# Kernel tuning notes

Measured on AMD Instinct MI355X. Metric: run time of the kernel, lower is better.

Reference implementation:

```python
import jax, jax.numpy as jnp
import numpy as np
from jax import lax

LEAK = 0.01   # nn.LeakyReLU default negative slope
EPS = 1e-5    # BatchNorm2d eps


def _conv(x, w, b, stride, pad):
    # torch Conv2d, NCHW / OIHW
    y = lax.conv_general_dilated(x, w, (stride, stride), [(pad, pad), (pad, pad)],
                                 dimension_numbers=('NCHW', 'OIHW', 'NCHW'))
    return y + b[None, :, None, None]


def _bn_lrelu(x, g, b):
    # BatchNorm2d in training mode (torch default): batch statistics over (N,H,W)
    m = jnp.mean(x, axis=(0, 2, 3), keepdims=True)
    v = jnp.var(x, axis=(0, 2, 3), keepdims=True)
    xn = (x - m) * lax.rsqrt(v + EPS) * g[None, :, None, None] + b[None, :, None, None]
    return jnp.where(xn >= 0, xn, LEAK * xn)


def _convt(x, w, b):
    # ConvTranspose2d with stride == kernel_size, padding=0: non-overlapping
    # k x k expansion of every pixel -> expressible as one einsum + reshape.
    # w: (Cin, Cout, k, k) (torch ConvTranspose2d layout)
    B, C, H, W = x.shape
    _, Co, k, _ = w.shape
    y = jnp.einsum('bchw,coij->bohiwj', x, w).reshape(B, Co, H * k, W * k)
    return y + b[None, :, None, None]


def setup_inputs() -> dict:
    key = jax.random.key(0)
    ks = iter(jax.random.split(key, 64))
    def rn(shape, s=0.05):
        return jax.random.normal(next(ks), shape, dtype=jnp.float32) * s
    d = {}
    d['x'] = jax.random.normal(next(ks), (16, 3, 128, 128), dtype=jnp.float32)
    enc_shapes = [(64, 3, 4, 4), (128, 64, 4, 4), (256, 128, 4, 4), (256, 256, 4, 4)]
    for i, s in enumerate(enc_shapes):
        d[f'enc_w{i}'] = rn(s)
        d[f'enc_b{i}'] = jnp.zeros((s[0],), jnp.float32)
    for i, c in enumerate([64, 128, 256]):
        d[f'ebn_g{i}'] = jnp.ones((c,), jnp.float32)
        d[f'ebn_b{i}'] = jnp.zeros((c,), jnp.float32)
    d['codebook'] = rn((512, 256), 1.0)  # (codebook_size, latent_dim)
    dec_shapes = [(256, 128, 4, 4), (128, 64, 2, 2), (64, 32, 2, 2)]
    for i, s in enumerate(dec_shapes):
        d[f'dec_w{i}'] = rn(s)
        d[f'dec_b{i}'] = jnp.zeros((s[1],), jnp.float32)
        d[f'dbn_g{i}'] = jnp.ones((s[1],), jnp.float32)
        d[f'dbn_b{i}'] = jnp.zeros((s[1],), jnp.float32)
    d['dec_w3'] = rn((3, 32, 1, 1))
    d['dec_b3'] = jnp.zeros((3,), jnp.float32)
    return d


def reference(x,
              enc_w0, enc_b0, ebn_g0, ebn_b0,
              enc_w1, enc_b1, ebn_g1, ebn_b1,
              enc_w2, enc_b2, ebn_g2, ebn_b2,
              enc_w3, enc_b3,
              codebook,
              dec_w0, dec_b0, dbn_g0, dbn_b0,
              dec_w1, dec_b1, dbn_g1, dbn_b1,
              dec_w2, dec_b2, dbn_g2, dbn_b2,
              dec_w3, dec_b3):
    # ---- encoder ----
    h = _bn_lrelu(_conv(x, enc_w0, enc_b0, 2, 1), ebn_g0, ebn_b0)   # (B,64,64,64)
    h = _bn_lrelu(_conv(h, enc_w1, enc_b1, 2, 1), ebn_g1, ebn_b1)   # (B,128,32,32)
    h = _bn_lrelu(_conv(h, enc_w2, enc_b2, 2, 1), ebn_g2, ebn_b2)   # (B,256,16,16)
    z = _conv(h, enc_w3, enc_b3, 2, 1)                               # (B,256,8,8)

    # ---- vector quantizer ----
    B, C, H, W = z.shape
    zf = z.transpose(0, 2, 3, 1).reshape(-1, C)                      # (BHW, C)
    # squared L2 distances to every codebook entry
    d2 = (jnp.sum(zf * zf, axis=-1, keepdims=True)
          - 2.0 * zf @ codebook.T
          + jnp.sum(codebook * codebook, axis=-1)[None, :])          # (BHW, K)
    idx = jnp.argmin(d2, axis=-1)                                    # (BHW,)
    min_d = jnp.min(d2, axis=-1)
    q = codebook[idx]                                                # (BHW, C)
    commitment_loss = jnp.mean((lax.stop_gradient(q) - zf) ** 2)
    codebook_loss = jnp.mean((q - lax.stop_gradient(zf)) ** 2)
    q_st = zf + lax.stop_gradient(q - zf)                            # straight-through
    qz = q_st.reshape(B, H, W, C).transpose(0, 3, 1, 2)              # (B,256,8,8)

    # ---- decoder ----
    h = _bn_lrelu(_convt(qz, dec_w0, dec_b0), dbn_g0, dbn_b0)        # (B,128,32,32)
    h = _bn_lrelu(_convt(h, dec_w1, dec_b1), dbn_g1, dbn_b1)         # (B,64,64,64)
    h = _bn_lrelu(_convt(h, dec_w2, dec_b2), dbn_g2, dbn_b2)         # (B,32,128,128)
    out = jnp.tanh(jnp.einsum('bchw,oc->bohw', h, dec_w3[:, :, 0, 0])
                   + dec_b3[None, :, None, None])                    # (B,3,128,128)

    return (out, commitment_loss, codebook_loss,
            idx.reshape(B, H, W), min_d.reshape(B, H, W))
```

## Files before the change

kernel.cpp:

```cpp
#include <hip/hip_runtime.h>
#include <math.h>

#define LEAK 0.01f

typedef __bf16 bf16x8 __attribute__((ext_vector_type(8)));
typedef float f32x4 __attribute__((ext_vector_type(4)));
typedef unsigned short ushort;
typedef unsigned int uint32;

struct HL { ushort h, l; };

__device__ inline HL split_bf16(float x) {
    unsigned u = __float_as_uint(x);
    unsigned hr = (u + 0x7FFFu + ((u >> 16) & 1u)) >> 16;
    float fh = __uint_as_float(hr << 16);
    float r = x - fh;
    unsigned v = __float_as_uint(r);
    unsigned lr = (v + 0x7FFFu + ((v >> 16) & 1u)) >> 16;
    HL out; out.h = (ushort)hr; out.l = (ushort)lr;
    return out;
}

template<int MODE>
__device__ inline void stage_load(float (&pv)[2][4], const float* __restrict__ Bf,
                                  int kbase, int n0, int tid,
                                  int Ci, int Hin, int Ho, int lgHo, int lgHW) {
    int nl = tid & 31, kg = tid >> 5;
    int n = n0 + nl;
#pragma unroll
    for (int r = 0; r < 2; ++r) {
        if (MODE == 0) {
            int k4 = kbase + (r << 5) + (kg << 2);
            int ic = k4 >> 4, kh = (k4 >> 2) & 3;
            int ow = n & (Ho - 1), oh = (n >> lgHo) & (Ho - 1), b = n >> (lgHo + lgHo);
            int ih = oh * 2 - 1 + kh;
            int ihc = ih < 0 ? 0 : (ih >= Hin ? Hin - 1 : ih);
            int iwb = ow * 2 - 1;
            size_t base = ((size_t)(b * Ci + ic) * Hin + ihc) * Hin;
#pragma unroll
            for (int e = 0; e < 4; ++e) {
                int iw = iwb + e;
                int iwc = iw < 0 ? 0 : (iw >= Hin ? Hin - 1 : iw);
                pv[r][e] = Bf[base + iwc];
            }
        } else {
            int c = kbase + (r << 5) + (kg << 2);
            int b = n >> lgHW, hw = n & ((1 << lgHW) - 1);
            size_t base = (((size_t)(b * Ci + c)) << lgHW) + hw;
            size_t str = (size_t)1 << lgHW;
#pragma unroll
            for (int e = 0; e < 4; ++e) pv[r][e] = Bf[base + e * str];
        }
    }
}

template<int MODE>
__global__ __launch_bounds__(256, 3) void gemm_mfma(
    const ushort* __restrict__ Ah, const ushort* __restrict__ Al,
    const float* __restrict__ Bf,
    const float* __restrict__ bnt, const float* __restrict__ gamma,
    const float* __restrict__ beta, float invN, int chanShift,
    const float* __restrict__ bias, float* __restrict__ P,
    int Mtiles, int Ntiles, int K, int Kslice, int KS, int outSize,
    int Ci, int Hin, int Co, int Ho, int lgHo,
    int lgHW, int lgHin, int lgCo, int lgk,
    float* __restrict__ statsBnt, const float* __restrict__ bnPart,
    int statsBank, int bntBankStride)
{
    __shared__ __align__(16) uint32 Bsp[32 * 68];
    __shared__ float scs[256], shs[256];

    int bid = blockIdx.x;
    int ntile = bid % Ntiles; bid /= Ntiles;
    int mtile = bid % Mtiles;
    int ks = bid / Mtiles;
    int tid = threadIdx.x;
    int lane = tid & 63, w = tid >> 6;
    int quad = lane >> 4, tl = lane & 15;
    int n0 = ntile << 5, m0 = mtile << 7, k0 = ks * Kslice;
    int Kt = K >> 5;

    bool useBN = (bnt != nullptr) || (bnPart != nullptr);
    int c0 = k0 >> chanShift;
    if (bnPart != nullptr) {
        int c = tid >> 2, qq = tid & 3;
        const float2* pp2 = (const float2*)(bnPart + c * 512) + qq * 64;
        float s = 0.f, s2 = 0.f;
#pragma unroll 8
        for (int p = 0; p < 64; ++p) { float2 v = pp2[p]; s += v.x; s2 += v.y; }
        scs[tid] = s; shs[tid] = s2;
        __syncthreads();
        float scale = 0.f, shift = 0.f;
        if (tid < 64) {
            float st = scs[tid * 4] + scs[tid * 4 + 1] + scs[tid * 4 + 2] + scs[tid * 4 + 3];
            float qt = shs[tid * 4] + shs[tid * 4 + 1] + shs[tid * 4 + 2] + shs[tid * 4 + 3];
            float m = st * invN;
            float var = qt * invN - m * m;
            scale = gamma[tid] * rsqrtf(var + 1e-5f);
            shift = beta[tid] - m * scale;
        }
        __syncthreads();
        if (tid < 64 && tid >= c0) { scs[tid - c0] = scale; shs[tid - c0] = shift; }
    } else if (bnt != nullptr) {
        int nch = Kslice >> chanShift;
        for (int c = tid; c < nch; c += 256) {
            float sm, sq;
            if (bntBankStride > 0) {
                sm = 0.f; sq = 0.f;
#pragma unroll
                for (int bk = 0; bk < 8; ++bk) {
                    sm += bnt[bk * bntBankStride + (c0 + c) * 2];
                    sq += bnt[bk * bntBankStride + (c0 + c) * 2 + 1];
                }
            } else {
                sm = bnt[(c0 + c) * 2];
                sq = bnt[(c0 + c) * 2 + 1];
            }
            float m = sm * invN;
            float var = sq * invN - m * m;
            float scale = gamma[c0 + c] * rsqrtf(var + 1e-5f);
            scs[c] = scale;
            shs[c] = beta[c0 + c] - m * scale;
        }
    }
    __syncthreads();

    f32x4 zero4 = {0.f, 0.f, 0.f, 0.f};
    f32x4 acc[2][2];
#pragma unroll
    for (int mt = 0; mt < 2; ++mt)
#pragma unroll
        for (int nt = 0; nt < 2; ++nt) acc[mt][nt] = zero4;

    if (MODE == 2) {
        const ushort* Bu = (const ushort*)Bf;
        for (int kc = 0; kc < Kslice; kc += 32) {
            int kbase = k0 + kc;
            int kt = kbase >> 5;
            bf16x8 afh[2], afl[2];
#pragma unroll
            for (int mt = 0; mt < 2; ++mt) {
                int mtAbs = (m0 >> 4) + (w << 1) + mt;
                size_t abase = (((size_t)mtAbs * Kt + kt) << 6) + lane;
                afh[mt] = *(const bf16x8*)(Ah + abase * 8);
                afl[mt] = *(const bf16x8*)(Al + abase * 8);
            }
            bf16x8 bfh[2], bfl[2];
#pragma unroll
            for (int nt = 0; nt < 2; ++nt) {
                int n = n0 + (nt << 4) + tl;
                size_t ba = (size_t)n * Ci + kbase + (quad << 3);
                bfh[nt] = *(const bf16x8*)(Bu + ba);
                bfl[nt] = *(const bf16x8*)(Bu + Ho + ba);
            }
#pragma unroll
            for (int mt = 0; mt < 2; ++mt)
#pragma unroll
                for (int nt = 0; nt < 2; ++nt) {
                    acc[mt][nt] = __builtin_amdgcn_mfma_f32_16x16x32_bf16(afh[mt], bfh[nt], acc[mt][nt], 0, 0, 0);
                    acc[mt][nt] = __builtin_amdgcn_mfma_f32_16x16x32_bf16(afh[mt], bfl[nt], acc[mt][nt], 0, 0, 0);
                    acc[mt][nt] = __builtin_amdgcn_mfma_f32_16x16x32_bf16(afl[mt], bfh[nt], acc[mt][nt], 0, 0, 0);
                }
        }
    } else {
        int nsteps = Kslice >> 6;
        float pvA[2][4], pvB[2][4];
        stage_load<MODE>(pvA, Bf, k0, n0, tid, Ci, Hin, Ho, lgHo, lgHW);
        if (nsteps > 1) stage_load<MODE>(pvB, Bf, k0 + 64, n0, tid, Ci, Hin, Ho, lgHo, lgHW);

        auto step = [&](float (&pv)[2][4], int sidx) {
            int kbase = k0 + (sidx << 6);
            int nl = tid & 31, kg = tid >> 5;
#pragma unroll
            for (int r = 0; r < 2; ++r) {
                int k4 = kbase + (r << 5) + (kg << 2);
                uint32 pk[4];
                if (MODE == 0) {
                    int ic = k4 >> 4, kh = (k4 >> 2) & 3;
                    int n = n0 + nl;
                    int ow = n & (Ho - 1), oh = (n >> lgHo) & (Ho - 1);
                    int ih = oh * 2 - 1 + kh;
                    bool rowok = (unsigned)ih < (unsigned)Hin;
                    int iwb = ow * 2 - 1;
                    float sc_ = useBN ? scs[ic - c0] : 0.f;
                    float sh_ = useBN ? shs[ic - c0] : 0.f;
#pragma unroll
                    for (int e = 0; e < 4; ++e) {
                        int iw = iwb + e;
                        bool ok = rowok && ((unsigned)iw < (unsigned)Hin);
                        float f = pv[r][e];
                        if (useBN) { f = f * sc_ + sh_; f = f >= 0.f ? f : LEAK * f; }
                        if (!ok) f = 0.f;
                        HL s = split_bf16(f);
                        pk[e] = ((uint32)s.h << 16) | s.l;
                    }
                } else {
#pragma unroll
                    for (int e = 0; e < 4; ++e) {
                        float f = pv[r][e];
                        if (useBN) {
                            int lc = k4 + e - k0;
                            f = f * scs[lc] + shs[lc];
                            f = f >= 0.f ? f : LEAK * f;
                        }
                        HL s = split_bf16(f);
                        pk[e] = ((uint32)s.h << 16) | s.l;
                    }
                }
                *(uint4*)&Bsp[nl * 68 + (r << 5) + (kg << 2)] = make_uint4(pk[0], pk[1], pk[2], pk[3]);
            }
            __syncthreads();

            if (sidx + 2 < nsteps)
                stage_load<MODE>(pv, Bf, kbase + 128, n0, tid, Ci, Hin, Ho, lgHo, lgHW);

#pragma unroll
            for (int sub = 0; sub < 2; ++sub) {
                int kt = (kbase >> 5) + sub;
                bf16x8 afh[2], afl[2];
#pragma unroll
                for (int mt = 0; mt < 2; ++mt) {
                    int mtAbs = (m0 >> 4) + (w << 1) + mt;
                    size_t abase = (((size_t)mtAbs * Kt + kt) << 6) + lane;
                    afh[mt] = *(const bf16x8*)(Ah + abase * 8);
                    afl[mt] = *(const bf16x8*)(Al + abase * 8);
                }
                bf16x8 bfh[2], bfl[2];
#pragma unroll
                for (int nt = 0; nt < 2; ++nt) {
                    int base = ((nt << 4) + tl) * 68 + (sub << 5) + (quad << 3);
                    uint4 ua = *(const uint4*)&Bsp[base];
                    uint4 ub = *(const uint4*)&Bsp[base + 4];
                    union { uint32 u[4]; bf16x8 v; } H, L;
                    H.u[0] = __builtin_amdgcn_perm(ua.y, ua.x, 0x07060302u);
                    H.u[1] = __builtin_amdgcn_perm(ua.w, ua.z, 0x07060302u);
                    H.u[2] = __builtin_amdgcn_perm(ub.y, ub.x, 0x07060302u);
                    H.u[3] = __builtin_amdgcn_perm(ub.w, ub.z, 0x07060302u);
                    L.u[0] = __builtin_amdgcn_perm(ua.y, ua.x, 0x05040100u);
                    L.u[1] = __builtin_amdgcn_perm(ua.w, ua.z, 0x05040100u);
                    L.u[2] = __builtin_amdgcn_perm(ub.y, ub.x, 0x05040100u);
                    L.u[3] = __builtin_amdgcn_perm(ub.w, ub.z, 0x05040100u);
                    bfh[nt] = H.v; bfl[nt] = L.v;
                }
#pragma unroll
                for (int mt = 0; mt < 2; ++mt)
#pragma unroll
                    for (int nt = 0; nt < 2; ++nt) {
                        acc[mt][nt] = __builtin_amdgcn_mfma_f32_16x16x32_bf16(afh[mt], bfh[nt], acc[mt][nt], 0, 0, 0);
                        acc[mt][nt] = __builtin_amdgcn_mfma_f32_16x16x32_bf16(afh[mt], bfl[nt], acc[mt][nt], 0, 0, 0);
                        acc[mt][nt] = __builtin_amdgcn_mfma_f32_16x16x32_bf16(afl[mt], bfh[nt], acc[mt][nt], 0, 0, 0);
                    }
            }
            __syncthreads();
        };

        for (int s = 0; s < nsteps; s += 2) {
            step(pvA, s);
            if (s + 1 < nsteps) step(pvB, s + 1);
        }
    }

    bool doStats = (statsBnt != nullptr);
    if (doStats) {
        if (tid < 2 * Co) scs[tid] = 0.f;
        __syncthreads();
    }
    float ssum[2][4] = {{0.f,0.f,0.f,0.f},{0.f,0.f,0.f,0.f}};
    float ssq [2][4] = {{0.f,0.f,0.f,0.f},{0.f,0.f,0.f,0.f}};
    float* dst = P + (size_t)ks * outSize;
    if (MODE == 0) {
#pragma unroll
        for (int nt = 0; nt < 2; ++nt) {
            int n = n0 + (nt << 4) + tl;
            int ow = n & (Ho - 1), oh = (n >> lgHo) & (Ho - 1), b = n >> (lgHo + lgHo);
#pragma unroll
            for (int mt = 0; mt < 2; ++mt) {
                int mb = m0 + (w << 5) + (mt << 4) + (quad << 2);
#pragma unroll
                for (int r = 0; r < 4; ++r) {
                    int oc = mb + r;
                    float v = acc[mt][nt][r];
                    if (KS == 1) v += bias[oc];
                    if (doStats) { ssum[mt][r] += v; ssq[mt][r] += v * v; }
                    dst[((size_t)(b * Co + oc) * Ho + oh) * Ho + ow] = v;
                }
            }
        }
    } else {
        int kf = 1 << lgk;
        int Ho2 = Hin << lgk;
#pragma unroll
        for (int nt = 0; nt < 2; ++nt) {
            int n = n0 + (nt << 4) + tl;
            int b = n >> lgHW, hw = n & ((1 << lgHW) - 1);
            int h = hw >> lgHin, wp = hw & (Hin - 1);
#pragma unroll
            for (int mt = 0; mt < 2; ++mt) {
                int mb = m0 + (w << 5) + (mt << 4) + (quad << 2);
#pragma unroll
                for (int r = 0; r < 4; ++r) {
                    int m = mb + r;
                    int o = m & (Co - 1), ij = m >> lgCo;
                    int ii = ij >> lgk, jj = ij & (kf - 1);
                    float v = acc[mt][nt][r];
                    if (KS == 1) v += bias[o];
                    if (doStats) { ssum[mt][r] += v; ssq[mt][r] += v * v; }
                    dst[((size_t)(b * Co + o) * Ho2 + (h << lgk) + ii) * Ho2 + (wp << lgk) + jj] = v;
                }
            }
        }
    }
    if (doStats) {
#pragma unroll
        for (int mt = 0; mt < 2; ++mt)
#pragma unroll
            for (int r = 0; r < 4; ++r) {
                float s = ssum[mt][r], q2 = ssq[mt][r];
#pragma unroll
                for (int m2 = 1; m2 < 16; m2 <<= 1) {
                    s  += __shfl_xor(s,  m2);
                    q2 += __shfl_xor(q2, m2);
                }
                if (tl == 0) {
                    int m = m0 + (w << 5) + (mt << 4) + (quad << 2) + r;
                    int o = (MODE == 0) ? m : (m & (Co - 1));
                    atomicAdd(&scs[o * 2],     s);
                    atomicAdd(&scs[o * 2 + 1], q2);
                }
            }
        __syncthreads();
        float* sb = statsBnt + (blockIdx.x & 7) * statsBank;
        if (tid < 2 * Co) atomicAdd(&sb[tid], scs[tid]);
    }
}

__device__ inline int fragaddr(int m, int k, int K) {
    return ((((m >> 4) * (K >> 5) + (k >> 5)) << 9) | (((k >> 3) & 3) << 7) | ((m & 15) << 3) | (k & 7));
}

#define OUT_CL   786432
#define OUT_CB   786433
#define OUT_IDX  786434
#define OUT_MIND 787458

__device__ void conv_body(int bid, int tid,
                          const float* __restrict__ x, const float* __restrict__ w,
                          const float* __restrict__ bias, float* __restrict__ P,
                          float* __restrict__ pst, float (&cst)[4][16])
{
    const int Ci = 3, Hin = 128, Co = 64, Ho = 64, OCT = 8;
    int ntile = (16 * Ho * Ho) >> 8;
    int tile = bid % ntile;
    int og = bid / ntile;
    int oc0 = og * OCT;

    int px = (tile << 8) + tid;
    int ow = px % Ho; int t = px / Ho;
    int oh = t % Ho;  int b = t / Ho;

    int off[16]; float fm[16];
    int ih0 = oh * 2 - 1, iw0 = ow * 2 - 1;
#pragma unroll
    for (int kh = 0; kh < 4; ++kh)
#pragma unroll
        for (int kw = 0; kw < 4; ++kw) {
            int ih = ih0 + kh, iw = iw0 + kw;
            bool ok = (ih >= 0) && (ih < Hin) && (iw >= 0) && (iw < Hin);
            int ihc = ih < 0 ? 0 : (ih >= Hin ? Hin - 1 : ih);
            int iwc = iw < 0 ? 0 : (iw >= Hin ? Hin - 1 : iw);
            off[kh * 4 + kw] = ihc * Hin + iwc;
            fm[kh * 4 + kw] = ok ? 1.f : 0.f;
        }

    float acc[OCT];
#pragma unroll
    for (int u = 0; u < OCT; ++u) acc[u] = bias[oc0 + u];

    const float* xc = x + (size_t)b * Ci * Hin * Hin;
    const float* wi = w + (size_t)oc0 * Ci * 16;
    int HinHin = Hin * Hin;
    for (int ic = 0; ic < Ci; ++ic) {
        float xv[16];
#pragma unroll
        for (int q = 0; q < 16; ++q) xv[q] = xc[off[q]] * fm[q];
#pragma unroll
        for (int u = 0; u < OCT; ++u) {
            const float* wo = wi + (size_t)u * Ci * 16;
            float a = acc[u];
#pragma unroll
            for (int q = 0; q < 16; ++q) a += xv[q] * wo[q];
            acc[u] = a;
        }
        xc += HinHin;
        wi += 16;
    }
    size_t obase = (((size_t)b * Co + oc0) * Ho + oh) * Ho + ow;
    size_t opl = (size_t)Ho * Ho;
#pragma unroll
    for (int u = 0; u < OCT; ++u) P[obase + u * opl] = acc[u];

    float sv[OCT], qv[OCT];
#pragma unroll
    for (int u = 0; u < OCT; ++u) { sv[u] = acc[u]; qv[u] = acc[u] * acc[u]; }
#pragma unroll
    for (int m2 = 1; m2 < 64; m2 <<= 1)
#pragma unroll
        for (int u = 0; u < OCT; ++u) {
            sv[u] += __shfl_xor(sv[u], m2);
            qv[u] += __shfl_xor(qv[u], m2);
        }
    int lane = tid & 63, wv = tid >> 6;
    if (lane == 0) {
#pragma unroll
        for (int u = 0; u < OCT; ++u) { cst[wv][u * 2] = sv[u]; cst[wv][u * 2 + 1] = qv[u]; }
    }
    __syncthreads();
    if (tid < 2 * OCT) {
        float v = cst[0][tid] + cst[1][tid] + cst[2][tid] + cst[3][tid];
        pst[(oc0 + (tid >> 1)) * 512 + tile * 2 + (tid & 1)] = v;
    }
}

__global__ void prologue(const float* __restrict__ w1, const float* __restrict__ w2,
                         const float* __restrict__ w3, const float* __restrict__ d0,
                         const float* __restrict__ d1, const float* __restrict__ d2,
                         ushort* __restrict__ WH, ushort* __restrict__ WL,
                         const float* __restrict__ cb, float* __restrict__ cbT,
                         float* __restrict__ bnt, float* __restrict__ dout,
                         const float* __restrict__ x, const float* __restrict__ w0,
                         const float* __restrict__ b0, float* __restrict__ Y0,
                         float* __restrict__ pst) {
    __shared__ float cst[4][16];
    int blk = blockIdx.x;
    int tid = threadIdx.x;
    if (blk < 24) {
        bnt[blk * 256 + tid] = 0.f;
        if (blk == 0 && tid < 2) dout[OUT_CL + tid] = 0.f;
        return;
    }
    if (blk < 536) {
        int idx = (blk - 24) * 256 + tid;
        int k = idx & 511, c = idx >> 9;
        cbT[idx] = cb[k * 256 + c];
        return;
    }
    if (blk >= 9400) {
        conv_body(blk - 9400, tid, x, w0, b0, Y0, pst, cst);
        return;
    }
    int idx = (blk - 536) * 256 + tid;
    if (idx >= 2269184) return;
    float v; int dst;
    if (idx < 131072) {
        int m = idx >> 10, k = idx & 1023;
        v = w1[idx];
        dst = fragaddr(m, k, 1024);
    } else if (idx < 655360) {
        int i = idx - 131072;
        int m = i >> 11, k = i & 2047;
        v = w2[i];
        dst = 131072 + fragaddr(m, k, 2048);
    } else if (idx < 1703936) {
        int i = idx - 655360;
        int m = i >> 12, k = i & 4095;
        v = w3[i];
        dst = 655360 + fragaddr(m, k, 4096);
    } else if (idx < 2228224) {
        int i = idx - 1703936;
        int m = i >> 8, c = i & 255;
        int o = m & 127, ij = m >> 7;
        v = d0[((size_t)c * 128 + o) * 16 + ij];
        dst = 1703936 + fragaddr(m, c, 256);
    } else if (idx < 2260992) {
        int i = idx - 2228224;
        int m = i >> 7, c = i & 127;
        int o = m & 63, ij = m >> 6;
        v = d1[((size_t)c * 64 + o) * 4 + ij];
        dst = 2228224 + fragaddr(m, c, 128);
    } else {
        int i = idx - 2260992;
        int m = i >> 6, c = i & 63;
        int o = m & 31, ij = m >> 5;
        v = d2[((size_t)c * 32 + o) * 4 + ij];
        dst = 2260992 + fragaddr(m, c, 64);
    }
    HL s = split_bf16(v);
    WH[dst] = s.h; WL[dst] = s.l;
}

__global__ void reduce_bias_stats4(const float4* __restrict__ P, const float* __restrict__ bias,
                                   float4* __restrict__ y, float* __restrict__ bnt,
                                   int outSize4, int KS, int Co, int HW4, int nch) {
    int tid = threadIdx.x;
    int i = blockIdx.x * 256 + tid;
    int c = (i / HW4) % Co;
    float bv = bias[c];
    float4 s = make_float4(bv, bv, bv, bv);
    for (int ks = 0; ks < KS; ++ks) {
        float4 p = P[(size_t)ks * outSize4 + i];
        s.x += p.x; s.y += p.y; s.z += p.z; s.w += p.w;
    }
    y[i] = s;
    float ls  = s.x + s.y + s.z + s.w;
    float ls2 = s.x * s.x + s.y * s.y + s.z * s.z + s.w * s.w;
    __shared__ float as[16], aq[16];
    if (tid < 16) { as[tid] = 0.f; aq[tid] = 0.f; }
    __syncthreads();
    int c0 = ((blockIdx.x * 256) / HW4) % Co;
    atomicAdd(&as[c - c0], ls);
    atomicAdd(&aq[c - c0], ls2);
    __syncthreads();
    if (tid < nch) {
        atomicAdd(&bnt[(c0 + tid) * 2],     as[tid]);
        atomicAdd(&bnt[(c0 + tid) * 2 + 1], aq[tid]);
    }
}

__global__ void vq_main(const float* __restrict__ Pz, const float* __restrict__ b3,
                        const float* __restrict__ cbT, const float* __restrict__ cb,
                        ushort* __restrict__ qhl, float* __restrict__ dout) {
    int r0 = blockIdx.x * 4;
    int tid = threadIdx.x;
    int lane = tid & 63, w = tid >> 6;

    __shared__ __align__(16) float zT[256][4];
    __shared__ float wred[4][4];
    __shared__ float zn2s[4];
    __shared__ float wbd[4][4];
    __shared__ int   wbi[4][4];
    __shared__ int   bestsh[4];
    __shared__ float bestd[4];

    int b = r0 >> 6, s0 = r0 & 63;
    size_t zi = ((size_t)(b * 256 + tid)) * 64 + s0;
    float bv = b3[tid];
    float4 zv = make_float4(bv, bv, bv, bv);
    const float4* pp = (const float4*)Pz + (zi >> 2);
#pragma unroll
    for (int ks = 0; ks < 16; ++ks) {
        float4 p = pp[(size_t)ks * 65536];
        zv.x += p.x; zv.y += p.y; zv.z += p.z; zv.w += p.w;
    }
    *(float4*)&zT[tid][0] = zv;

    float p0 = zv.x * zv.x, p1 = zv.y * zv.y, p2 = zv.z * zv.z, p3 = zv.w * zv.w;
#pragma unroll
    for (int m2 = 1; m2 < 64; m2 <<= 1) {
        p0 += __shfl_xor(p0, m2); p1 += __shfl_xor(p1, m2);
        p2 += __shfl_xor(p2, m2); p3 += __shfl_xor(p3, m2);
    }
    if (lane == 0) { wred[w][0] = p0; wred[w][1] = p1; wred[w][2] = p2; wred[w][3] = p3; }
    __syncthreads();
    if (tid < 4) zn2s[tid] = wred[0][tid] + wred[1][tid] + wred[2][tid] + wred[3][tid];
    __syncthreads();

    float d0[4], d1[4];
#pragma unroll
    for (int rr = 0; rr < 4; ++rr) { d0[rr] = 0.f; d1[rr] = 0.f; }
    float cn0 = 0.f, cn1 = 0.f;
#pragma unroll 4
    for (int c = 0; c < 256; ++c) {
        float cv0 = cbT[c * 512 + tid];
        float cv1 = cbT[c * 512 + 256 + tid];
        cn0 += cv0 * cv0;
        cn1 += cv1 * cv1;
        float4 za = *(const float4*)&zT[c][0];
        d0[0] += za.x * cv0; d1[0] += za.x * cv1;
        d0[1] += za.y * cv0; d1[1] += za.y * cv1;
        d0[2] += za.z * cv0; d1[2] += za.z * cv1;
        d0[3] += za.w * cv0; d1[3] += za.w * cv1;
    }

#pragma unroll
    for (int rr = 0; rr < 4; ++rr) {
        float dist0 = zn2s[rr] - 2.f * d0[rr] + cn0;
        float dist1 = zn2s[rr] - 2.f * d1[rr] + cn1;
        float bd = dist0; int bi = tid;
        if (dist1 < bd) { bd = dist1; bi = tid + 256; }
#pragma unroll
        for (int m2 = 1; m2 < 64; m2 <<= 1) {
            float od = __shfl_xor(bd, m2); int oi = __shfl_xor(bi, m2);
            if (od < bd || (od == bd && oi < bi)) { bd = od; bi = oi; }
        }
        if (lane == 0) { wbd[w][rr] = bd; wbi[w][rr] = bi; }
    }
    __syncthreads();
    if (tid < 4) {
        float bd = wbd[0][tid]; int bi = wbi[0][tid];
#pragma unroll
        for (int ww = 1; ww < 4; ++ww) {
            float od = wbd[ww][tid]; int oi = wbi[ww][tid];
            if (od < bd || (od == bd && oi < bi)) { bd = od; bi = oi; }
        }
        bestsh[tid] = bi; bestd[tid] = bd;
        dout[OUT_IDX + r0 + tid]  = (float)bi;
        dout[OUT_MIND + r0 + tid] = bd;
    }
    __syncthreads();

#pragma unroll
    for (int rr = 0; rr < 4; ++rr) {
        float v = cb[(size_t)bestsh[rr] * 256 + tid];
        HL s = split_bf16(v);
        size_t o = (size_t)(r0 + rr) * 256 + tid;
        qhl[o]          = s.h;
        qhl[262144 + o] = s.l;
    }
    if (tid == 0) {
        float ls = (bestd[0] + bestd[1] + bestd[2] + bestd[3]) * (1.f / 262144.f);
        atomicAdd(&dout[OUT_CL], ls);
        atomicAdd(&dout[OUT_CB], ls);
    }
}

__global__ void final_conv_tanh(const float* __restrict__ hbuf, const float* __restrict__ bnt,
                                const float* __restrict__ g, const float* __restrict__ bt,
                                const float* __restrict__ w3, const float* __restrict__ b3,
                                float* __restrict__ out) {
    __shared__ float sc[32], sh[32], sw[96];
    int tid = threadIdx.x;
    if (tid < 32) {
        float sm = 0.f, sq = 0.f;
#pragma unroll
        for (int bk = 0; bk < 8; ++bk) {
            sm += bnt[bk * 64 + tid * 2];
            sq += bnt[bk * 64 + tid * 2 + 1];
        }
        float m = sm * (1.f / 262144.f);
        float var = sq * (1.f / 262144.f) - m * m;
        float scale = g[tid] * rsqrtf(var + 1e-5f);
        sc[tid] = scale;
        sh[tid] = bt[tid] - m * scale;
    }
    if (tid < 96) sw[tid] = w3[tid];
    __syncthreads();
    int idx = blockIdx.x * 256 + tid;
    int hw4 = idx & 4095;
    int b   = idx >> 12;
    const float4* hp = (const float4*)hbuf + ((size_t)b * 32) * 4096 + hw4;
    float b0 = b3[0], b1 = b3[1], b2 = b3[2];
    float4 a0 = make_float4(b0, b0, b0, b0);
    float4 a1 = make_float4(b1, b1, b1, b1);
    float4 a2 = make_float4(b2, b2, b2, b2);
#pragma unroll 8
    for (int c = 0; c < 32; ++c) {
        float4 v = hp[(size_t)c * 4096];
        float scv = sc[c], shv = sh[c];
        float vx = v.x * scv + shv; vx = vx >= 0.f ? vx : LEAK * vx;
        float vy = v.y * scv + shv; vy = vy >= 0.f ? vy : LEAK * vy;
        float vz = v.z * scv + shv; vz = vz >= 0.f ? vz : LEAK * vz;
        float vw = v.w * scv + shv; vw = vw >= 0.f ? vw : LEAK * vw;
        float w0 = sw[c], w1 = sw[32 + c], w2 = sw[64 + c];
        a0.x += vx * w0; a0.y += vy * w0; a0.z += vz * w0; a0.w += vw * w0;
        a1.x += vx * w1; a1.y += vy * w1; a1.z += vz * w1; a1.w += vw * w1;
        a2.x += vx * w2; a2.y += vy * w2; a2.z += vz * w2; a2.w += vw * w2;
    }
    float4* op = (float4*)out;
    size_t ob = ((size_t)b * 3) * 4096 + hw4;
    op[ob]            = make_float4(tanhf(a0.x), tanhf(a0.y), tanhf(a0.z), tanhf(a0.w));
    op[ob + 4096]     = make_float4(tanhf(a1.x), tanhf(a1.y), tanhf(a1.z), tanhf(a1.w));
    op[ob + 2 * 4096] = make_float4(tanhf(a2.x), tanhf(a2.y), tanhf(a2.z), tanhf(a2.w));
}

extern "C" void kernel_launch(void* const* d_in, const int* in_sizes, int n_in,
                              void* d_out, int out_size, void* d_ws, size_t ws_size,
                              hipStream_t stream) {
    const float* x      = (const float*)d_in[0];
    const float* enc_w0 = (const float*)d_in[1];
    const float* enc_b0 = (const float*)d_in[2];
    const float* enc_w1 = (const float*)d_in[3];
    const float* enc_b1 = (const float*)d_in[4];
    const float* enc_w2 = (const float*)d_in[5];
    const float* enc_b2 = (const float*)d_in[6];
    const float* enc_w3 = (const float*)d_in[7];
    const float* enc_b3 = (const float*)d_in[8];
    const float* ebn_g0 = (const float*)d_in[9];
    const float* ebn_b0 = (const float*)d_in[10];
    const float* ebn_g1 = (const float*)d_in[11];
    const float* ebn_b1 = (const float*)d_in[12];
    const float* ebn_g2 = (const float*)d_in[13];
    const float* ebn_b2 = (const float*)d_in[14];
    const float* cb     = (const float*)d_in[15];
    const float* dec_w0 = (const float*)d_in[16];
    const float* dec_b0 = (const float*)d_in[17];
    const float* dbn_g0 = (const float*)d_in[18];
    const float* dbn_b0 = (const float*)d_in[19];
    const float* dec_w1 = (const float*)d_in[20];
    const float* dec_b1 = (const float*)d_in[21];
    const float* dbn_g1 = (const float*)d_in[22];
    const float* dbn_b1 = (const float*)d_in[23];
    const float* dec_w2 = (const float*)d_in[24];
    const float* dec_b2 = (const float*)d_in[25];
    const float* dbn_g2 = (const float*)d_in[26];
    const float* dbn_b2 = (const float*)d_in[27];
    const float* dec_w3 = (const float*)d_in[28];
    const float* dec_b3 = (const float*)d_in[29];

    float* out = (float*)d_out;
    float* ws  = (float*)d_ws;

    float*  Y0   = ws;
    float*  Y1   = ws + 4194304;
    float*  Y2   = ws + 6291456;
    float*  PST  = ws + 7340032;
    float*  QHL  = ws + 7602176;
    ushort* WH   = (ushort*)(ws + 7864320);
    ushort* WL   = (ushort*)(ws + 8998912);
    float*  CBT  = ws + 10133504;
    float*  BNT  = ws + 10264576;
    float*  PART = ws + 10270720;
    float*  D0   = ws + 18659328;
    float*  D1   = ws + 20756480;
    float*  D2   = ws + 24950784;

    dim3 blk(256);

    prologue<<<11448, blk, 0, stream>>>(enc_w1, enc_w2, enc_w3, dec_w0, dec_w1, dec_w2,
                                        WH, WL, cb, CBT, BNT, out,
                                        x, enc_w0, enc_b0, Y0, PST);

    gemm_mfma<0><<<512, blk, 0, stream>>>(WH, WL, Y0,
        nullptr, ebn_g0, ebn_b0, 1.f / 65536.f, 4, enc_b1, Y1,
        1, 512, 1024, 1024, 1, 0, 64, 64, 128, 32, 5, 0, 0, 0, 0, BNT, PST, 256, 0);

    gemm_mfma<0><<<1024, blk, 0, stream>>>(WH + 131072, WL + 131072, Y1,
        BNT, ebn_g1, ebn_b1, 1.f / 16384.f, 4, enc_b2, PART,
        2, 128, 2048, 512, 4, 1048576, 128, 32, 256, 16, 4, 0, 0, 0, 0, nullptr, nullptr, 0, 256);
    reduce_bias_stats4<<<1024, blk, 0, stream>>>((const float4*)PART, enc_b2, (float4*)Y2,
                                                 BNT + 2048, 262144, 4, 256, 64, 4);

    gemm_mfma<0><<<1024, blk, 0, stream>>>(WH + 655360, WL + 655360, Y2,
        BNT + 2048, ebn_g2, ebn_b2, 1.f / 4096.f, 4, enc_b3, PART,
        2, 32, 4096, 256, 16, 262144, 256, 16, 256, 8, 3, 0, 0, 0, 0, nullptr, nullptr, 0, 0);

    vq_main<<<256, blk, 0, stream>>>(PART, enc_b3, CBT, cb, (ushort*)QHL, out);

    gemm_mfma<2><<<512, blk, 0, stream>>>(WH + 1703936, WL + 1703936, QHL,
        nullptr, nullptr, nullptr, 0.f, 0, dec_b0, D0,
        16, 32, 256, 256, 1, 0, 256, 8, 128, 262144, 0, 6, 3, 7, 2, BNT + 2560, nullptr, 256, 0);

    gemm_mfma<1><<<1024, blk, 0, stream>>>(WH + 2228224, WL + 2228224, D0,
        BNT + 2560, dbn_g0, dbn_b0, 1.f / 16384.f, 0, dec_b1, D1,
        2, 512, 128, 128, 1, 0, 128, 32, 64, 0, 0, 10, 5, 6, 1, BNT + 4608, nullptr, 128, 256);

    gemm_mfma<1><<<2048, blk, 0, stream>>>(WH + 2260992, WL + 2260992, D1,
        BNT + 4608, dbn_g1, dbn_b1, 1.f / 65536.f, 0, dec_b2, D2,
        1, 2048, 64, 64, 1, 0, 64, 64, 32, 0, 0, 12, 6, 5, 1, BNT + 5632, nullptr, 64, 128);

    final_conv_tanh<<<256, blk, 0, stream>>>(D2, BNT + 5632, dbn_g2, dbn_b2, dec_w3, dec_b3, out);
}
```

Measured before the change: 364.6 us.

## Template GEMM on M-tile multiplier, double M tile for mid layers, prefetch A

```diff
diff --git a/kernel.cpp b/kernel.cpp
--- a/kernel.cpp
+++ b/kernel.cpp
@@ -54,7 +54,7 @@
     }
 }
 
-template<int MODE>
+template<int MODE, int MT>
 __global__ __launch_bounds__(256, 3) void gemm_mfma(
     const ushort* __restrict__ Ah, const ushort* __restrict__ Al,
     const float* __restrict__ Bf,
@@ -77,7 +77,7 @@
     int tid = threadIdx.x;
     int lane = tid & 63, w = tid >> 6;
     int quad = lane >> 4, tl = lane & 15;
-    int n0 = ntile << 5, m0 = mtile << 7, k0 = ks * Kslice;
+    int n0 = ntile << 5, m0 = mtile * (128 * MT), k0 = ks * Kslice;
     int Kt = K >> 5;
 
     bool useBN = (bnt != nullptr) || (bnPart != nullptr);
@@ -126,9 +126,9 @@
     __syncthreads();
 
     f32x4 zero4 = {0.f, 0.f, 0.f, 0.f};
-    f32x4 acc[2][2];
-#pragma unroll
-    for (int mt = 0; mt < 2; ++mt)
+    f32x4 acc[2 * MT][2];
+#pragma unroll
+    for (int mt = 0; mt < 2 * MT; ++mt)
 #pragma unroll
         for (int nt = 0; nt < 2; ++nt) acc[mt][nt] = zero4;
 
@@ -137,10 +137,10 @@
         for (int kc = 0; kc < Kslice; kc += 32) {
             int kbase = k0 + kc;
             int kt = kbase >> 5;
-            bf16x8 afh[2], afl[2];
-#pragma unroll
-            for (int mt = 0; mt < 2; ++mt) {
-                int mtAbs = (m0 >> 4) + (w << 1) + mt;
+            bf16x8 afh[2 * MT], afl[2 * MT];
+#pragma unroll
+            for (int mt = 0; mt < 2 * MT; ++mt) {
+                int mtAbs = (m0 >> 4) + w * (2 * MT) + mt;
                 size_t abase = (((size_t)mtAbs * Kt + kt) << 6) + lane;
                 afh[mt] = *(const bf16x8*)(Ah + abase * 8);
                 afl[mt] = *(const bf16x8*)(Al + abase * 8);
@@ -153,14 +153,16 @@
                 bfh[nt] = *(const bf16x8*)(Bu + ba);
                 bfl[nt] = *(const bf16x8*)(Bu + Ho + ba);
             }
-#pragma unroll
-            for (int mt = 0; mt < 2; ++mt)
+            __builtin_amdgcn_s_setprio(1);
+#pragma unroll
+            for (int mt = 0; mt < 2 * MT; ++mt)
 #pragma unroll
                 for (int nt = 0; nt < 2; ++nt) {
                     acc[mt][nt] = __builtin_amdgcn_mfma_f32_16x16x32_bf16(afh[mt], bfh[nt], acc[mt][nt], 0, 0, 0);
                     acc[mt][nt] = __builtin_amdgcn_mfma_f32_16x16x32_bf16(afh[mt], bfl[nt], acc[mt][nt], 0, 0, 0);
                     acc[mt][nt] = __builtin_amdgcn_mfma_f32_16x16x32_bf16(afl[mt], bfh[nt], acc[mt][nt], 0, 0, 0);
                 }
+            __builtin_amdgcn_s_setprio(0);
         }
     } else {
         int nsteps = Kslice >> 6;
@@ -211,19 +213,39 @@
             }
             __syncthreads();
 
+            bf16x8 afhP[2][2], aflP[2][2];
+            if constexpr (MT == 1) {
+#pragma unroll
+                for (int sub = 0; sub < 2; ++sub) {
+                    int kt = (kbase >> 5) + sub;
+#pragma unroll
+                    for (int mt = 0; mt < 2; ++mt) {
+                        int mtAbs = (m0 >> 4) + (w << 1) + mt;
+                        size_t abase = (((size_t)mtAbs * Kt + kt) << 6) + lane;
+                        afhP[sub][mt] = *(const bf16x8*)(Ah + abase * 8);
+                        aflP[sub][mt] = *(const bf16x8*)(Al + abase * 8);
+                    }
+                }
+            }
+
             if (sidx + 2 < nsteps)
                 stage_load<MODE>(pv, Bf, kbase + 128, n0, tid, Ci, Hin, Ho, lgHo, lgHW);
 
 #pragma unroll
             for (int sub = 0; sub < 2; ++sub) {
-                int kt = (kbase >> 5) + sub;
-                bf16x8 afh[2], afl[2];
-#pragma unroll
-                for (int mt = 0; mt < 2; ++mt) {
-                    int mtAbs = (m0 >> 4) + (w << 1) + mt;
-                    size_t abase = (((size_t)mtAbs * Kt + kt) << 6) + lane;
-                    afh[mt] = *(const bf16x8*)(Ah + abase * 8);
-                    afl[mt] = *(const bf16x8*)(Al + abase * 8);
+                bf16x8 afh[2 * MT], afl[2 * MT];
+                if constexpr (MT == 1) {
+#pragma unroll
+                    for (int mt = 0; mt < 2; ++mt) { afh[mt] = afhP[sub][mt]; afl[mt] = aflP[sub][mt]; }
+                } else {
+                    int kt = (kbase >> 5) + sub;
+#pragma unroll
+                    for (int mt = 0; mt < 2 * MT; ++mt) {
+                        int mtAbs = (m0 >> 4) + w * (2 * MT) + mt;
+                        size_t abase = (((size_t)mtAbs * Kt + kt) << 6) + lane;
+                        afh[mt] = *(const bf16x8*)(Ah + abase * 8);
+                        afl[mt] = *(const bf16x8*)(Al + abase * 8);
+                    }
                 }
                 bf16x8 bfh[2], bfl[2];
 #pragma unroll
@@ -242,14 +264,16 @@
                     L.u[3] = __builtin_amdgcn_perm(ub.w, ub.z, 0x05040100u);
                     bfh[nt] = H.v; bfl[nt] = L.v;
                 }
-#pragma unroll
-                for (int mt = 0; mt < 2; ++mt)
+                __builtin_amdgcn_s_setprio(1);
+#pragma unroll
+                for (int mt = 0; mt < 2 * MT; ++mt)
 #pragma unroll
                     for (int nt = 0; nt < 2; ++nt) {
                         acc[mt][nt] = __builtin_amdgcn_mfma_f32_16x16x32_bf16(afh[mt], bfh[nt], acc[mt][nt], 0, 0, 0);
                         acc[mt][nt] = __builtin_amdgcn_mfma_f32_16x16x32_bf16(afh[mt], bfl[nt], acc[mt][nt], 0, 0, 0);
                         acc[mt][nt] = __builtin_amdgcn_mfma_f32_16x16x32_bf16(afl[mt], bfh[nt], acc[mt][nt], 0, 0, 0);
                     }
+                __builtin_amdgcn_s_setprio(0);
             }
             __syncthreads();
         };
@@ -265,8 +289,8 @@
         if (tid < 2 * Co) scs[tid] = 0.f;
         __syncthreads();
     }
-    float ssum[2][4] = {{0.f,0.f,0.f,0.f},{0.f,0.f,0.f,0.f}};
-    float ssq [2][4] = {{0.f,0.f,0.f,0.f},{0.f,0.f,0.f,0.f}};
+    float ssum[2 * MT][4] = {};
+    float ssq [2 * MT][4] = {};
     float* dst = P + (size_t)ks * outSize;
     if (MODE == 0) {
 #pragma unroll
@@ -274,8 +298,8 @@
             int n = n0 + (nt << 4) + tl;
             int ow = n & (Ho - 1), oh = (n >> lgHo) & (Ho - 1), b = n >> (lgHo + lgHo);
 #pragma unroll
-            for (int mt = 0; mt < 2; ++mt) {
-                int mb = m0 + (w << 5) + (mt << 4) + (quad << 2);
+            for (int mt = 0; mt < 2 * MT; ++mt) {
+                int mb = m0 + w * (32 * MT) + (mt << 4) + (quad << 2);
 #pragma unroll
                 for (int r = 0; r < 4; ++r) {
                     int oc = mb + r;
@@ -295,8 +319,8 @@
             int b = n >> lgHW, hw = n & ((1 << lgHW) - 1);
             int h = hw >> lgHin, wp = hw & (Hin - 1);
 #pragma unroll
-            for (int mt = 0; mt < 2; ++mt) {
-                int mb = m0 + (w << 5) + (mt << 4) + (quad << 2);
+            for (int mt = 0; mt < 2 * MT; ++mt) {
+                int mb = m0 + w * (32 * MT) + (mt << 4) + (quad << 2);
 #pragma unroll
                 for (int r = 0; r < 4; ++r) {
                     int m = mb + r;
@@ -312,7 +336,7 @@
     }
     if (doStats) {
 #pragma unroll
-        for (int mt = 0; mt < 2; ++mt)
+        for (int mt = 0; mt < 2 * MT; ++mt)
 #pragma unroll
             for (int r = 0; r < 4; ++r) {
                 float s = ssum[mt][r], q2 = ssq[mt][r];
@@ -322,7 +346,7 @@
                     q2 += __shfl_xor(q2, m2);
                 }
                 if (tl == 0) {
-                    int m = m0 + (w << 5) + (mt << 4) + (quad << 2) + r;
+                    int m = m0 + w * (32 * MT) + (mt << 4) + (quad << 2) + r;
                     int o = (MODE == 0) ? m : (m & (Co - 1));
                     atomicAdd(&scs[o * 2],     s);
                     atomicAdd(&scs[o * 2 + 1], q2);
@@ -719,31 +743,31 @@
                                         WH, WL, cb, CBT, BNT, out,
                                         x, enc_w0, enc_b0, Y0, PST);
 
-    gemm_mfma<0><<<512, blk, 0, stream>>>(WH, WL, Y0,
+    gemm_mfma<0, 1><<<512, blk, 0, stream>>>(WH, WL, Y0,
         nullptr, ebn_g0, ebn_b0, 1.f / 65536.f, 4, enc_b1, Y1,
         1, 512, 1024, 1024, 1, 0, 64, 64, 128, 32, 5, 0, 0, 0, 0, BNT, PST, 256, 0);
 
-    gemm_mfma<0><<<1024, blk, 0, stream>>>(WH + 131072, WL + 131072, Y1,
+    gemm_mfma<0, 2><<<512, blk, 0, stream>>>(WH + 131072, WL + 131072, Y1,
         BNT, ebn_g1, ebn_b1, 1.f / 16384.f, 4, enc_b2, PART,
-        2, 128, 2048, 512, 4, 1048576, 128, 32, 256, 16, 4, 0, 0, 0, 0, nullptr, nullptr, 0, 256);
+        1, 128, 2048, 512, 4, 1048576, 128, 32, 256, 16, 4, 0, 0, 0, 0, nullptr, nullptr, 0, 256);
     reduce_bias_stats4<<<1024, blk, 0, stream>>>((const float4*)PART, enc_b2, (float4*)Y2,
                                                  BNT + 2048, 262144, 4, 256, 64, 4);
 
-    gemm_mfma<0><<<1024, blk, 0, stream>>>(WH + 655360, WL + 655360, Y2,
+    gemm_mfma<0, 2><<<512, blk, 0, stream>>>(WH + 655360, WL + 655360, Y2,
         BNT + 2048, ebn_g2, ebn_b2, 1.f / 4096.f, 4, enc_b3, PART,
-        2, 32, 4096, 256, 16, 262144, 256, 16, 256, 8, 3, 0, 0, 0, 0, nullptr, nullptr, 0, 0);
+        1, 32, 4096, 256, 16, 262144, 256, 16, 256, 8, 3, 0, 0, 0, 0, nullptr, nullptr, 0, 0);
 
     vq_main<<<256, blk, 0, stream>>>(PART, enc_b3, CBT, cb, (ushort*)QHL, out);
 
-    gemm_mfma<2><<<512, blk, 0, stream>>>(WH + 1703936, WL + 1703936, QHL,
+    gemm_mfma<2, 1><<<512, blk, 0, stream>>>(WH + 1703936, WL + 1703936, QHL,
         nullptr, nullptr, nullptr, 0.f, 0, dec_b0, D0,
         16, 32, 256, 256, 1, 0, 256, 8, 128, 262144, 0, 6, 3, 7, 2, BNT + 2560, nullptr, 256, 0);
 
-    gemm_mfma<1><<<1024, blk, 0, stream>>>(WH + 2228224, WL + 2228224, D0,
+    gemm_mfma<1, 2><<<512, blk, 0, stream>>>(WH + 2228224, WL + 2228224, D0,
         BNT + 2560, dbn_g0, dbn_b0, 1.f / 16384.f, 0, dec_b1, D1,
-        2, 512, 128, 128, 1, 0, 128, 32, 64, 0, 0, 10, 5, 6, 1, BNT + 4608, nullptr, 128, 256);
-
-    gemm_mfma<1><<<2048, blk, 0, stream>>>(WH + 2260992, WL + 2260992, D1,
+        1, 512, 128, 128, 1, 0, 128, 32, 64, 0, 0, 10, 5, 6, 1, BNT + 4608, nullptr, 128, 256);
+
+    gemm_mfma<1, 1><<<2048, blk, 0, stream>>>(WH + 2260992, WL + 2260992, D1,
         BNT + 4608, dbn_g1, dbn_b1, 1.f / 65536.f, 0, dec_b2, D2,
         1, 2048, 64, 64, 1, 0, 64, 64, 32, 0, 0, 12, 6, 5, 1, BNT + 5632, nullptr, 64, 128);
 
```

Result: faster. 351.9 us (-3.5%).
